# Kernel optimization log

Measured on AMD Instinct MI355X. Metric: run time of the kernel, lower is better.

Reference implementation:

```python
import jax, jax.numpy as jnp
import numpy as np

B, L = 256, 128            # batch_size, max_len
VOCAB, EMB = 50000, 448
POS_NUM, POS_SZ = 128, 32
UNITS = 512                # gru_units == EMB + 2*POS_SZ (BiGRU input dim)
NUM_CLASSES = 53


def setup_inputs() -> dict:
    key = jax.random.key(0)
    ks = jax.random.split(key, 16)
    s = 0.05
    return {
        "input_word": jax.random.randint(ks[0], (B, L), 0, VOCAB),
        "input_pos1": jax.random.randint(ks[1], (B, L), 0, POS_NUM),
        "input_pos2": jax.random.randint(ks[2], (B, L), 0, POS_NUM),
        "word_emb": jax.random.normal(ks[3], (VOCAB, EMB), jnp.float32) * s,
        "pos_emb": jax.random.normal(ks[4], (POS_NUM, POS_SZ), jnp.float32) * s,
        # Keras GRU (reset_after=True): kernel [D,3U], recurrent_kernel [U,3U], bias [2,3U]
        "gru_kernel_f": jax.random.normal(ks[5], (UNITS, 3 * UNITS), jnp.float32) * s,
        "gru_rkernel_f": jax.random.normal(ks[6], (UNITS, 3 * UNITS), jnp.float32) * s,
        "gru_bias_f": jax.random.normal(ks[7], (2, 3 * UNITS), jnp.float32) * s,
        "gru_kernel_b": jax.random.normal(ks[8], (UNITS, 3 * UNITS), jnp.float32) * s,
        "gru_rkernel_b": jax.random.normal(ks[9], (UNITS, 3 * UNITS), jnp.float32) * s,
        "gru_bias_b": jax.random.normal(ks[10], (2, 3 * UNITS), jnp.float32) * s,
        "attention_w": jax.random.normal(ks[11], (UNITS, 1), jnp.float32) * s,
        "sen_a": jax.random.normal(ks[12], (UNITS,), jnp.float32) * s,
        "sen_r": jax.random.normal(ks[13], (UNITS, 1), jnp.float32) * s,
        "sen_d": jax.random.normal(ks[14], (NUM_CLASSES,), jnp.float32) * s,
        "sen_s": jax.random.normal(ks[15], (NUM_CLASSES, UNITS), jnp.float32) * s,
    }


def _gru(x, kernel, rkernel, bias):
    """Keras GRU, reset_after=True, tanh/sigmoid activations. x: [B,L,D] -> [B,L,U]."""
    bi, br = bias[0], bias[1]
    # precompute input projections for all timesteps: [B,L,3U]
    xp = jnp.einsum('bld,dh->blh', x, kernel) + bi
    U = rkernel.shape[0]
    def step(h, xt):  # xt: [B,3U]
        rec = h @ rkernel + br
        xz, xr, xh = jnp.split(xt, 3, axis=-1)
        rz, rr, rh = jnp.split(rec, 3, axis=-1)
        z = jax.nn.sigmoid(xz + rz)
        r = jax.nn.sigmoid(xr + rr)
        hh = jnp.tanh(xh + r * rh)
        h_new = z * h + (1.0 - z) * hh
        return h_new, h_new
    h0 = jnp.zeros((x.shape[0], U), x.dtype)
    _, hs = jax.lax.scan(step, h0, jnp.swapaxes(xp, 0, 1))  # [L,B,U]
    return jnp.swapaxes(hs, 0, 1)


def _bigru(x, kf, rf, bf, kb, rb, bb):
    """Bidirectional GRU, merge_mode='sum'."""
    fwd = _gru(x, kf, rf, bf)
    bwd = _gru(x[:, ::-1], kb, rb, bb)[:, ::-1]
    return fwd + bwd


def reference(input_word, input_pos1, input_pos2, word_emb, pos_emb,
              gru_kernel_f, gru_rkernel_f, gru_bias_f,
              gru_kernel_b, gru_rkernel_b, gru_bias_b,
              attention_w, sen_a, sen_r, sen_d, sen_s):
    # embedding lookups; embedding of reversed indices == time-reverse of embedding
    we = word_emb[input_word]        # [B,L,EMB]
    p1 = pos_emb[input_pos1]         # [B,L,POS_SZ]
    p2 = pos_emb[input_pos2]
    x_f = jnp.concatenate([we, p1, p2], axis=-1)  # [B,L,UNITS]
    x_b = x_f[:, ::-1]
    # same BiGRU (shared weights) applied to forward and reversed inputs, summed
    h = (_bigru(x_f, gru_kernel_f, gru_rkernel_f, gru_bias_f,
                gru_kernel_b, gru_rkernel_b, gru_bias_b)
         + _bigru(x_b, gru_kernel_f, gru_rkernel_f, gru_bias_f,
                  gru_kernel_b, gru_rkernel_b, gru_bias_b))  # dropout = identity (inference)
    inputs_h = jnp.tanh(h)  # [B,L,U]
    # word attention: scalar score per token, softmax over sequence
    scores = (inputs_h @ attention_w)[..., 0]           # [B,L]
    w_alpha = jax.nn.softmax(scores, axis=-1)           # [B,L]
    w_att_r = jnp.einsum('bl,blu->bu', w_alpha, h)      # weighted sum of PRE-tanh h
    # sentence attention (vectorized over what was a per-sample Python loop)
    r = jnp.tanh(w_att_r)                               # [B,U]
    e = ((r * sen_a) @ sen_r)[:, 0]                     # [B]
    a = jax.nn.softmax(e, axis=0)[:, None]              # softmax across the batch, [B,1]
    s_c = a * r                                         # [B,U]
    logits = s_c @ sen_s.T + sen_d                      # [B,C]
    return jax.nn.softmax(logits, axis=-1)
```

## Files before the change

### kernel.cpp

```cpp
#include <hip/hip_runtime.h>
#include <cstddef>
#include <cstdint>

#define BATCH 256
#define SEQL  128
#define BL    (BATCH * SEQL)
#define DIM   512
#define N3    1536
#define NCLS  53
#define HGN   (4 * 256 * 512)

typedef float f32x4 __attribute__((ext_vector_type(4)));
typedef short s16x8 __attribute__((ext_vector_type(8)));
typedef short s16x4 __attribute__((ext_vector_type(4)));

__device__ __forceinline__ float bf2f(unsigned short u) {
    union { unsigned int i; float f; } v; v.i = ((unsigned int)u) << 16; return v.f;
}
__device__ __forceinline__ unsigned short f2bf(float f) {
    union { float f; unsigned int i; } v; v.f = f;
    unsigned int x = v.i;
    return (unsigned short)((x + 0x7fffu + ((x >> 16) & 1u)) >> 16);
}
__device__ __forceinline__ float wave_sum(float v) {
    #pragma unroll
    for (int m = 32; m > 0; m >>= 1) v += __shfl_xor(v, m);
    return v;
}
__device__ __forceinline__ float wave_max(float v) {
    #pragma unroll
    for (int m = 32; m > 0; m >>= 1) v = fmaxf(v, __shfl_xor(v, m));
    return v;
}
__device__ __forceinline__ float sigmoidf(float x) { return 1.0f / (1.0f + expf(-x)); }

__global__ __launch_bounds__(64) void zero_bar_kernel(int* bar) {
    bar[threadIdx.x * 32] = 0;
}

__global__ __launch_bounds__(256) void transpose_kernel(const float* __restrict__ W,
                                                        unsigned short* __restrict__ Wt) {
    __shared__ float tile[32][33];
    int tx = threadIdx.x & 31, ty = threadIdx.x >> 5;
    int n0 = blockIdx.x * 32, k0 = blockIdx.y * 32;
    #pragma unroll
    for (int r = 0; r < 4; ++r) {
        int kl = ty + r * 8;
        tile[kl][tx] = W[(size_t)(k0 + kl) * N3 + n0 + tx];
    }
    __syncthreads();
    #pragma unroll
    for (int r = 0; r < 4; ++r) {
        int nl = ty + r * 8;
        Wt[(size_t)(n0 + nl) * DIM + k0 + tx] = f2bf(tile[tx][nl]);
    }
}

__global__ __launch_bounds__(64) void gather_kernel(const int* __restrict__ iw,
                                                    const int* __restrict__ ip1,
                                                    const int* __restrict__ ip2,
                                                    const float* __restrict__ wemb,
                                                    const float* __restrict__ pemb,
                                                    unsigned short* __restrict__ X) {
    int row = blockIdx.x;
    int tid = threadIdx.x;
    int w = iw[row], p1 = ip1[row], p2 = ip2[row];
    int e0 = tid * 8;
    s16x8 o;
    #pragma unroll
    for (int j = 0; j < 8; ++j) {
        int e = e0 + j;
        float f;
        if (e < 448)      f = wemb[(size_t)w * 448 + e];
        else if (e < 480) f = pemb[p1 * 32 + (e - 448)];
        else              f = pemb[p2 * 32 + (e - 480)];
        o[j] = (short)f2bf(f);
    }
    *(s16x8*)(X + (size_t)row * DIM + e0) = o;
}

__global__ __launch_bounds__(256, 4) void xq_gemm_kernel(const unsigned short* __restrict__ X,
                                                         const unsigned short* __restrict__ Ktf,
                                                         const unsigned short* __restrict__ Ktb,
                                                         unsigned short* __restrict__ XQf,
                                                         unsigned short* __restrict__ XQb) {
    int dir = blockIdx.z & 1;
    int ns  = blockIdx.z >> 1;
    const unsigned short* Kt = dir ? Ktb : Ktf;
    unsigned short* XQ = dir ? XQb : XQf;
    int l    = blockIdx.x;
    int bblk = blockIdx.y;
    int b0 = bblk * 32;
    int u0 = ns * 128;

    __shared__ alignas(16) unsigned short As[32 * 512];
    int tid = threadIdx.x;
    #pragma unroll
    for (int it = 0; it < 8; ++it) {
        int lin = (it * 256 + tid) * 16;
        int row = lin >> 10;
        int off = lin & 1023;
        const char* src = (const char*)X + ((((size_t)(b0 + row)) * 128 + l) << 10) + off;
        *(s16x8*)((char*)As + (lin ^ ((row & 7) << 4))) = *(const s16x8*)src;
    }
    __syncthreads();

    int lane = tid & 63, wv = tid >> 6;
    int mi = wv >> 1, wc = wv & 1;
    int lr = lane & 15, lg = lane >> 4;

    f32x4 acc[3][4];
    #pragma unroll
    for (int g = 0; g < 3; ++g)
        #pragma unroll
        for (int ni = 0; ni < 4; ++ni) acc[g][ni] = (f32x4){0.f, 0.f, 0.f, 0.f};

    int ar = mi * 16 + lr;
    #pragma unroll 4
    for (int kk = 0; kk < 16; ++kk) {
        s16x8 a = *(const s16x8*)((const char*)As +
                    (((ar << 10) + (kk << 6) + (lg << 4)) ^ ((ar & 7) << 4)));
        #pragma unroll
        for (int g = 0; g < 3; ++g)
            #pragma unroll
            for (int ni = 0; ni < 4; ++ni) {
                int brow = g * 512 + u0 + wc * 64 + ni * 16 + lr;
                s16x8 b = *(const s16x8*)(Kt + ((size_t)brow << 9) + (kk << 5) + (lg << 3));
                acc[g][ni] = __builtin_amdgcn_mfma_f32_16x16x32_bf16(a, b, acc[g][ni], 0, 0, 0);
            }
    }

    int w_t = ns * 2 + wc;
    #pragma unroll
    for (int g = 0; g < 3; ++g)
        #pragma unroll
        for (int ni = 0; ni < 4; ++ni) {
            size_t base = (((size_t)l * 8 + bblk) * 8 + w_t) * 6144
                        + (size_t)((g * 4 + ni) * 2 + mi) * 256;
            s16x4 o;
            #pragma unroll
            for (int reg = 0; reg < 4; ++reg) o[reg] = (short)f2bf(acc[g][ni][reg]);
            *(s16x4*)(XQ + base + lane * 4) = o;
        }
}

__device__ __forceinline__ void group_barrier(int* cnt, int target) {
    __syncthreads();
    if (threadIdx.x == 0) {
        __hip_atomic_fetch_add(cnt, 1, __ATOMIC_RELEASE, __HIP_MEMORY_SCOPE_AGENT);
        while (__hip_atomic_load(cnt, __ATOMIC_RELAXED, __HIP_MEMORY_SCOPE_AGENT) < target)
            __builtin_amdgcn_s_sleep(1);
        __hip_atomic_fetch_add(cnt, 0, __ATOMIC_ACQUIRE, __HIP_MEMORY_SCOPE_AGENT);
    }
    __syncthreads();
}

__global__ __launch_bounds__(512, 2) void gru_coop2_kernel(
    const unsigned short* __restrict__ XQf, const unsigned short* __restrict__ XQb,
    const unsigned short* __restrict__ Btf, const unsigned short* __restrict__ Btb,
    const float* __restrict__ gbf, const float* __restrict__ gbb,
    unsigned short* __restrict__ Hg, int* __restrict__ bar,
    unsigned short* __restrict__ HA, unsigned short* __restrict__ HB,
    unsigned short* __restrict__ HC, unsigned short* __restrict__ HD) {
    int wg = blockIdx.x;
    int grp  = wg & 7;
    int run  = grp & 3;
    int rowh = grp >> 2;
    int uslc = wg >> 3;
    int* cnt = bar + grp * 32;
    const unsigned short* Bt = (run < 2) ? Btf : Btb;
    const unsigned short* XQ = (run < 2) ? XQf : XQb;
    const float* gb = (run < 2) ? gbf : gbb;
    unsigned short* Hout = (run == 0) ? HA : (run == 1) ? HB : (run == 2) ? HC : HD;
    bool revx = (run == 1 || run == 2);
    bool revo = (run >= 2);

    int tid = threadIdx.x;
    int lane = tid & 63, wv = tid >> 6;
    int lr = lane & 15, lg = lane >> 4;

    __shared__ alignas(16) unsigned short Ws[48 * 512];
    #pragma unroll
    for (int it = 0; it < 6; ++it) {
        int lin = (it * 512 + tid) * 16;
        int wrow = lin >> 10;
        int off = lin & 1023;
        int g = wrow >> 4, i = wrow & 15;
        const char* src = (const char*)Bt + (((size_t)(g * 512 + uslc * 16 + i)) << 10) + off;
        *(s16x8*)((char*)Ws + (lin ^ ((wrow & 7) << 4))) = *(const s16x8*)src;
    }

    int u_col = uslc * 16 + lr;
    float bZv  = gb[u_col] + gb[N3 + u_col];
    float bRv  = gb[512 + u_col] + gb[N3 + 512 + u_col];
    float bIHv = gb[1024 + u_col];
    float bRHv = gb[N3 + 1024 + u_col];

    int mrow0 = rowh * 128 + wv * 16;
    int arow  = mrow0 + lr;
    int bblk = rowh * 4 + (wv >> 1);
    int mi = wv & 1;
    int w_t = uslc >> 2, ni_t = uslc & 3;

    f32x4 hm = (f32x4){0.f, 0.f, 0.f, 0.f};
    #pragma unroll
    for (int reg = 0; reg < 4; ++reg) {
        int row = mrow0 + lg * 4 + reg;
        Hg[((size_t)(run * 256 + row) << 9) + u_col] = 0;
    }
    int target = 32;
    group_barrier(cnt, target); target += 32;

    for (int t = 0; t < SEQL; ++t) {
        const unsigned short* cur = Hg + (size_t)(t & 1) * HGN;
        unsigned short* nxt = Hg + (size_t)((t + 1) & 1) * HGN;
        int tx = revx ? (127 - t) : t;
        int th = revo ? (127 - t) : t;

        const unsigned short* xqb = XQ + (((size_t)tx * 8 + bblk) * 8 + w_t) * 6144
                                       + (size_t)lane * 4;
        s16x4 xqz = *(const s16x4*)(xqb + ((0 * 4 + ni_t) * 2 + mi) * 256);
        s16x4 xqr = *(const s16x4*)(xqb + ((1 * 4 + ni_t) * 2 + mi) * 256);
        s16x4 xqh = *(const s16x4*)(xqb + ((2 * 4 + ni_t) * 2 + mi) * 256);

        const unsigned short* ap = cur + ((size_t)(run * 256 + arow) << 9) + (lg << 3);

        f32x4 aZ = (f32x4){0.f, 0.f, 0.f, 0.f};
        f32x4 aR = (f32x4){0.f, 0.f, 0.f, 0.f};
        f32x4 aH = (f32x4){0.f, 0.f, 0.f, 0.f};
        const char* wsb = (const char*)Ws;
        #pragma unroll 8
        for (int kk = 0; kk < 16; ++kk) {
            s16x8 a = *(const s16x8*)(ap + (kk << 5));
            int sw = (lr & 7) << 4;
            s16x8 bz = *(const s16x8*)(wsb + ((((0 * 16 + lr) << 10) + (kk << 6) + (lg << 4)) ^ sw));
            s16x8 br = *(const s16x8*)(wsb + ((((1 * 16 + lr) << 10) + (kk << 6) + (lg << 4)) ^ sw));
            s16x8 bh = *(const s16x8*)(wsb + ((((2 * 16 + lr) << 10) + (kk << 6) + (lg << 4)) ^ sw));
            aZ = __builtin_amdgcn_mfma_f32_16x16x32_bf16(a, bz, aZ, 0, 0, 0);
            aR = __builtin_amdgcn_mfma_f32_16x16x32_bf16(a, br, aR, 0, 0, 0);
            aH = __builtin_amdgcn_mfma_f32_16x16x32_bf16(a, bh, aH, 0, 0, 0);
        }

        #pragma unroll
        for (int reg = 0; reg < 4; ++reg) {
            int row = mrow0 + lg * 4 + reg;
            float z  = sigmoidf(bf2f((unsigned short)xqz[reg]) + bZv + aZ[reg]);
            float rg = sigmoidf(bf2f((unsigned short)xqr[reg]) + bRv + aR[reg]);
            float hh = tanhf(bf2f((unsigned short)xqh[reg]) + bIHv + rg * (aH[reg] + bRHv));
            float hn = z * hm[reg] + (1.0f - z) * hh;
            hm[reg] = hn;
            unsigned short hb = f2bf(hn);
            nxt[((size_t)(run * 256 + row) << 9) + u_col] = hb;
            Hout[(((size_t)row * SEQL) + th) * DIM + u_col] = hb;
        }
        if (t < SEQL - 1) { group_barrier(cnt, target); target += 32; }
    }
}

__global__ __launch_bounds__(64) void attn_scores_kernel(const unsigned short* __restrict__ HA,
                                                         const unsigned short* __restrict__ HB,
                                                         const unsigned short* __restrict__ HC,
                                                         const unsigned short* __restrict__ HD,
                                                         const float* __restrict__ attw,
                                                         float* __restrict__ scores) {
    int bl = blockIdx.x;
    int lane = threadIdx.x;
    size_t base = (size_t)bl * DIM + lane * 8;
    s16x8 h1 = *(const s16x8*)(HA + base);
    s16x8 h2 = *(const s16x8*)(HB + base);
    s16x8 h3 = *(const s16x8*)(HC + base);
    s16x8 h4 = *(const s16x8*)(HD + base);
    float s = 0.0f;
    #pragma unroll
    for (int j = 0; j < 8; ++j) {
        float hv = bf2f((unsigned short)h1[j]) + bf2f((unsigned short)h2[j])
                 + bf2f((unsigned short)h3[j]) + bf2f((unsigned short)h4[j]);
        s += tanhf(hv) * attw[lane * 8 + j];
    }
    s = wave_sum(s);
    if (lane == 0) scores[bl] = s;
}

__global__ __launch_bounds__(64) void softmax_l_kernel(const float* __restrict__ scores,
                                                       float* __restrict__ alpha) {
    int b = blockIdx.x, lane = threadIdx.x;
    float s0 = scores[b * SEQL + lane];
    float s1 = scores[b * SEQL + 64 + lane];
    float m = wave_max(fmaxf(s0, s1));
    float e0 = expf(s0 - m), e1 = expf(s1 - m);
    float sum = wave_sum(e0 + e1);
    alpha[b * SEQL + lane] = e0 / sum;
    alpha[b * SEQL + 64 + lane] = e1 / sum;
}

__global__ __launch_bounds__(512) void attn_apply_kernel(const unsigned short* __restrict__ HA,
                                                         const unsigned short* __restrict__ HB,
                                                         const unsigned short* __restrict__ HC,
                                                         const unsigned short* __restrict__ HD,
                                                         const float* __restrict__ alpha,
                                                         const float* __restrict__ sena,
                                                         const float* __restrict__ senr,
                                                         float* __restrict__ rbuf,
                                                         float* __restrict__ ebuf) {
    int b = blockIdx.x, tid = threadIdx.x;
    __shared__ float al[SEQL];
    __shared__ float red[8];
    if (tid < SEQL) al[tid] = alpha[b * SEQL + tid];
    __syncthreads();
    float w0 = 0.0f;
    #pragma unroll 2
    for (int l = 0; l < SEQL; ++l) {
        size_t base = ((size_t)b * SEQL + l) * DIM + tid;
        w0 += al[l] * (bf2f(HA[base]) + bf2f(HB[base]) + bf2f(HC[base]) + bf2f(HD[base]));
    }
    float r0 = tanhf(w0);
    rbuf[(size_t)b * DIM + tid] = r0;
    float pv = r0 * sena[tid] * senr[tid];
    pv = wave_sum(pv);
    if ((tid & 63) == 0) red[tid >> 6] = pv;
    __syncthreads();
    if (tid == 0) {
        float s = 0.0f;
        #pragma unroll
        for (int i = 0; i < 8; ++i) s += red[i];
        ebuf[b] = s;
    }
}

__global__ __launch_bounds__(64) void batch_softmax_kernel(const float* __restrict__ ebuf,
                                                           float* __restrict__ abuf) {
    int lane = threadIdx.x;
    float v0 = ebuf[lane], v1 = ebuf[64 + lane], v2 = ebuf[128 + lane], v3 = ebuf[192 + lane];
    float m = wave_max(fmaxf(fmaxf(v0, v1), fmaxf(v2, v3)));
    float e0 = expf(v0 - m), e1 = expf(v1 - m), e2 = expf(v2 - m), e3 = expf(v3 - m);
    float s = wave_sum(e0 + e1 + e2 + e3);
    abuf[lane] = e0 / s; abuf[64 + lane] = e1 / s;
    abuf[128 + lane] = e2 / s; abuf[192 + lane] = e3 / s;
}

__global__ __launch_bounds__(64) void final_out_kernel(const float* __restrict__ rbuf,
                                                       const float* __restrict__ abuf,
                                                       const float* __restrict__ sens,
                                                       const float* __restrict__ send,
                                                       float* __restrict__ out) {
    int b = blockIdx.x, lane = threadIdx.x;
    __shared__ float lg[NCLS];
    float ab = abuf[b];
    float rv[8];
    #pragma unroll
    for (int j = 0; j < 8; ++j) rv[j] = rbuf[(size_t)b * DIM + j * 64 + lane];
    for (int c = 0; c < NCLS; ++c) {
        float d = 0.0f;
        #pragma unroll
        for (int j = 0; j < 8; ++j) d += rv[j] * sens[(size_t)c * DIM + j * 64 + lane];
        d = wave_sum(d);
        if (lane == 0) lg[c] = ab * d + send[c];
    }
    __syncthreads();
    float x = (lane < NCLS) ? lg[lane] : -3.0e38f;
    float m = wave_max(x);
    float ex = (lane < NCLS) ? expf(x - m) : 0.0f;
    float s = wave_sum(ex);
    if (lane < NCLS) out[b * NCLS + lane] = ex / s;
}

extern "C" void kernel_launch(void* const* d_in, const int* in_sizes, int n_in,
                              void* d_out, int out_size, void* d_ws, size_t ws_size,
                              hipStream_t stream) {
    (void)in_sizes; (void)n_in; (void)out_size; (void)ws_size;
    const int*   iw   = (const int*)d_in[0];
    const int*   ip1  = (const int*)d_in[1];
    const int*   ip2  = (const int*)d_in[2];
    const float* wemb = (const float*)d_in[3];
    const float* pemb = (const float*)d_in[4];
    const float* kf   = (const float*)d_in[5];
    const float* rf   = (const float*)d_in[6];
    const float* gbf  = (const float*)d_in[7];
    const float* kb   = (const float*)d_in[8];
    const float* rb   = (const float*)d_in[9];
    const float* gbb  = (const float*)d_in[10];
    const float* attw = (const float*)d_in[11];
    const float* sena = (const float*)d_in[12];
    const float* senr = (const float*)d_in[13];
    const float* send = (const float*)d_in[14];
    const float* sens = (const float*)d_in[15];
    float* out = (float*)d_out;

    char* p = (char*)d_ws;
    auto take = [&](size_t n) { char* q = p; p += ((n + 255) & ~(size_t)255); return q; };
    unsigned short* X    = (unsigned short*)take((size_t)BL * DIM * 2);
    unsigned short* Ktf  = (unsigned short*)take((size_t)N3 * DIM * 2);
    unsigned short* Ktb  = (unsigned short*)take((size_t)N3 * DIM * 2);
    unsigned short* Btf  = (unsigned short*)take((size_t)N3 * DIM * 2);
    unsigned short* Btb  = (unsigned short*)take((size_t)N3 * DIM * 2);
    unsigned short* XQf  = (unsigned short*)take((size_t)BL * N3 * 2);
    unsigned short* XQb  = (unsigned short*)take((size_t)BL * N3 * 2);
    unsigned short* HB   = (unsigned short*)take((size_t)BL * DIM * 2);
    unsigned short* HC   = (unsigned short*)take((size_t)BL * DIM * 2);
    unsigned short* HD   = (unsigned short*)take((size_t)BL * DIM * 2);
    unsigned short* Hg   = (unsigned short*)take((size_t)2 * HGN * 2);
    int*            bar  = (int*)take((size_t)64 * 32 * 4);
    float* scores = (float*)take((size_t)BL * 4);
    float* alpha  = (float*)take((size_t)BL * 4);
    float* rbuf   = (float*)take((size_t)BATCH * DIM * 4);
    float* ebuf   = (float*)take((size_t)BATCH * 4);
    float* abuf   = (float*)take((size_t)BATCH * 4);
    unsigned short* HA = X;

    zero_bar_kernel<<<1, 64, 0, stream>>>(bar);
    transpose_kernel<<<dim3(48, 16), 256, 0, stream>>>(kf, Ktf);
    transpose_kernel<<<dim3(48, 16), 256, 0, stream>>>(kb, Ktb);
    transpose_kernel<<<dim3(48, 16), 256, 0, stream>>>(rf, Btf);
    transpose_kernel<<<dim3(48, 16), 256, 0, stream>>>(rb, Btb);
    gather_kernel<<<BL, 64, 0, stream>>>(iw, ip1, ip2, wemb, pemb, X);

    xq_gemm_kernel<<<dim3(128, 8, 8), 256, 0, stream>>>(X, Ktf, Ktb, XQf, XQb);

    {
        const unsigned short* aXQf = XQf; const unsigned short* aXQb = XQb;
        const unsigned short* aBtf = Btf; const unsigned short* aBtb = Btb;
        const float* agbf = gbf; const float* agbb = gbb;
        unsigned short* aHg = Hg; int* abar = bar;
        unsigned short* aHA = HA; unsigned short* aHB = HB;
        unsigned short* aHC = HC; unsigned short* aHD = HD;
        void* args[] = { &aXQf, &aXQb, &aBtf, &aBtb, &agbf, &agbb,
                         &aHg, &abar, &aHA, &aHB, &aHC, &aHD };
        hipLaunchCooperativeKernel((void*)gru_coop2_kernel, dim3(256), dim3(512),
                                   args, 0, stream);
    }

    attn_scores_kernel<<<BL, 64, 0, stream>>>(HA, HB, HC, HD, attw, scores);
    softmax_l_kernel<<<BATCH, 64, 0, stream>>>(scores, alpha);
    attn_apply_kernel<<<BATCH, 512, 0, stream>>>(HA, HB, HC, HD, alpha, sena, senr, rbuf, ebuf);
    batch_softmax_kernel<<<1, 64, 0, stream>>>(ebuf, abuf);
    final_out_kernel<<<BATCH, 64, 0, stream>>>(rbuf, abuf, sens, send, out);
}
```

Baseline: 2.773 ms.

## Halve GRU block size, give each wave two M-tiles sharing B fragments

The cooperative GRU kernel now runs 256 threads per block instead of 512. Each wave computes two 16-row M tiles, so every LDS read of a recurrent-weight fragment feeds two MFMAs instead of one. The LDS weight layout is rewritten into a lane-major, MFMA-fragment order so each lane reads a contiguous 16-byte chunk without XOR swizzling. The intent is to cut LDS traffic and the per-block barrier cost, at the price of fewer waves to hide latency and more registers per thread.

```diff
diff --git a/kernel.cpp b/kernel.cpp
--- a/kernel.cpp
+++ b/kernel.cpp
@@ -155,7 +155,7 @@
     __syncthreads();
 }
 
-__global__ __launch_bounds__(512, 2) void gru_coop2_kernel(
+__global__ __launch_bounds__(256, 1) void gru_coop3_kernel(
     const unsigned short* __restrict__ XQf, const unsigned short* __restrict__ XQb,
     const unsigned short* __restrict__ Btf, const unsigned short* __restrict__ Btb,
     const float* __restrict__ gbf, const float* __restrict__ gbb,
@@ -181,13 +181,15 @@
 
     __shared__ alignas(16) unsigned short Ws[48 * 512];
     #pragma unroll
-    for (int it = 0; it < 6; ++it) {
-        int lin = (it * 512 + tid) * 16;
-        int wrow = lin >> 10;
-        int off = lin & 1023;
-        int g = wrow >> 4, i = wrow & 15;
-        const char* src = (const char*)Bt + (((size_t)(g * 512 + uslc * 16 + i)) << 10) + off;
-        *(s16x8*)((char*)Ws + (lin ^ ((wrow & 7) << 4))) = *(const s16x8*)src;
+    for (int it = 0; it < 12; ++it) {
+        int idx = it * 256 + tid;
+        int r  = idx & 15;
+        int lgs = (idx >> 4) & 3;
+        int kk = (idx >> 6) & 15;
+        int g  = idx >> 10;
+        const char* src = (const char*)Bt + (((size_t)(g * 512 + uslc * 16 + r)) << 10)
+                                          + (kk << 6) + (lgs << 4);
+        *(s16x8*)((char*)Ws + idx * 16) = *(const s16x8*)src;
     }
 
     int u_col = uslc * 16 + lr;
@@ -196,17 +198,17 @@
     float bIHv = gb[1024 + u_col];
     float bRHv = gb[N3 + 1024 + u_col];
 
-    int mrow0 = rowh * 128 + wv * 16;
-    int arow  = mrow0 + lr;
-    int bblk = rowh * 4 + (wv >> 1);
-    int mi = wv & 1;
+    int m0a = rowh * 128 + wv * 32;
+    int m0b = m0a + 16;
+    int bblk = rowh * 4 + wv;
     int w_t = uslc >> 2, ni_t = uslc & 3;
 
-    f32x4 hm = (f32x4){0.f, 0.f, 0.f, 0.f};
+    f32x4 hma = (f32x4){0.f, 0.f, 0.f, 0.f};
+    f32x4 hmb = (f32x4){0.f, 0.f, 0.f, 0.f};
     #pragma unroll
     for (int reg = 0; reg < 4; ++reg) {
-        int row = mrow0 + lg * 4 + reg;
-        Hg[((size_t)(run * 256 + row) << 9) + u_col] = 0;
+        Hg[((size_t)(run * 256 + m0a + lg * 4 + reg) << 9) + u_col] = 0;
+        Hg[((size_t)(run * 256 + m0b + lg * 4 + reg) << 9) + u_col] = 0;
     }
     int target = 32;
     group_barrier(cnt, target); target += 32;
@@ -219,39 +221,59 @@
 
         const unsigned short* xqb = XQ + (((size_t)tx * 8 + bblk) * 8 + w_t) * 6144
                                        + (size_t)lane * 4;
-        s16x4 xqz = *(const s16x4*)(xqb + ((0 * 4 + ni_t) * 2 + mi) * 256);
-        s16x4 xqr = *(const s16x4*)(xqb + ((1 * 4 + ni_t) * 2 + mi) * 256);
-        s16x4 xqh = *(const s16x4*)(xqb + ((2 * 4 + ni_t) * 2 + mi) * 256);
-
-        const unsigned short* ap = cur + ((size_t)(run * 256 + arow) << 9) + (lg << 3);
-
-        f32x4 aZ = (f32x4){0.f, 0.f, 0.f, 0.f};
-        f32x4 aR = (f32x4){0.f, 0.f, 0.f, 0.f};
-        f32x4 aH = (f32x4){0.f, 0.f, 0.f, 0.f};
-        const char* wsb = (const char*)Ws;
+        s16x4 xqza = *(const s16x4*)(xqb + ((0 * 4 + ni_t) * 2 + 0) * 256);
+        s16x4 xqzb = *(const s16x4*)(xqb + ((0 * 4 + ni_t) * 2 + 1) * 256);
+        s16x4 xqra = *(const s16x4*)(xqb + ((1 * 4 + ni_t) * 2 + 0) * 256);
+        s16x4 xqrb = *(const s16x4*)(xqb + ((1 * 4 + ni_t) * 2 + 1) * 256);
+        s16x4 xqha = *(const s16x4*)(xqb + ((2 * 4 + ni_t) * 2 + 0) * 256);
+        s16x4 xqhb = *(const s16x4*)(xqb + ((2 * 4 + ni_t) * 2 + 1) * 256);
+
+        const char* apa = (const char*)cur + (((size_t)(run * 256 + m0a + lr)) << 10) + (lg << 4);
+        const char* apb = (const char*)cur + (((size_t)(run * 256 + m0b + lr)) << 10) + (lg << 4);
+        const char* wsb = (const char*)Ws + (size_t)lane * 16;
+
+        f32x4 aZ0 = {0.f,0.f,0.f,0.f}, aZ1 = {0.f,0.f,0.f,0.f};
+        f32x4 aR0 = {0.f,0.f,0.f,0.f}, aR1 = {0.f,0.f,0.f,0.f};
+        f32x4 aH0 = {0.f,0.f,0.f,0.f}, aH1 = {0.f,0.f,0.f,0.f};
         #pragma unroll 8
         for (int kk = 0; kk < 16; ++kk) {
-            s16x8 a = *(const s16x8*)(ap + (kk << 5));
-            int sw = (lr & 7) << 4;
-            s16x8 bz = *(const s16x8*)(wsb + ((((0 * 16 + lr) << 10) + (kk << 6) + (lg << 4)) ^ sw));
-            s16x8 br = *(const s16x8*)(wsb + ((((1 * 16 + lr) << 10) + (kk << 6) + (lg << 4)) ^ sw));
-            s16x8 bh = *(const s16x8*)(wsb + ((((2 * 16 + lr) << 10) + (kk << 6) + (lg << 4)) ^ sw));
-            aZ = __builtin_amdgcn_mfma_f32_16x16x32_bf16(a, bz, aZ, 0, 0, 0);
-            aR = __builtin_amdgcn_mfma_f32_16x16x32_bf16(a, br, aR, 0, 0, 0);
-            aH = __builtin_amdgcn_mfma_f32_16x16x32_bf16(a, bh, aH, 0, 0, 0);
+            s16x8 a0 = *(const s16x8*)(apa + (kk << 6));
+            s16x8 a1 = *(const s16x8*)(apb + (kk << 6));
+            s16x8 bz = *(const s16x8*)(wsb + ((0 * 16 + kk) << 10));
+            s16x8 br = *(const s16x8*)(wsb + ((1 * 16 + kk) << 10));
+            s16x8 bh = *(const s16x8*)(wsb + ((2 * 16 + kk) << 10));
+            aZ0 = __builtin_amdgcn_mfma_f32_16x16x32_bf16(a0, bz, aZ0, 0, 0, 0);
+            aZ1 = __builtin_amdgcn_mfma_f32_16x16x32_bf16(a1, bz, aZ1, 0, 0, 0);
+            aR0 = __builtin_amdgcn_mfma_f32_16x16x32_bf16(a0, br, aR0, 0, 0, 0);
+            aR1 = __builtin_amdgcn_mfma_f32_16x16x32_bf16(a1, br, aR1, 0, 0, 0);
+            aH0 = __builtin_amdgcn_mfma_f32_16x16x32_bf16(a0, bh, aH0, 0, 0, 0);
+            aH1 = __builtin_amdgcn_mfma_f32_16x16x32_bf16(a1, bh, aH1, 0, 0, 0);
         }
 
         #pragma unroll
         for (int reg = 0; reg < 4; ++reg) {
-            int row = mrow0 + lg * 4 + reg;
-            float z  = sigmoidf(bf2f((unsigned short)xqz[reg]) + bZv + aZ[reg]);
-            float rg = sigmoidf(bf2f((unsigned short)xqr[reg]) + bRv + aR[reg]);
-            float hh = tanhf(bf2f((unsigned short)xqh[reg]) + bIHv + rg * (aH[reg] + bRHv));
-            float hn = z * hm[reg] + (1.0f - z) * hh;
-            hm[reg] = hn;
-            unsigned short hb = f2bf(hn);
-            nxt[((size_t)(run * 256 + row) << 9) + u_col] = hb;
-            Hout[(((size_t)row * SEQL) + th) * DIM + u_col] = hb;
+            {
+                int row = m0a + lg * 4 + reg;
+                float z  = sigmoidf(bf2f((unsigned short)xqza[reg]) + bZv + aZ0[reg]);
+                float rg = sigmoidf(bf2f((unsigned short)xqra[reg]) + bRv + aR0[reg]);
+                float hh = tanhf(bf2f((unsigned short)xqha[reg]) + bIHv + rg * (aH0[reg] + bRHv));
+                float hn = z * hma[reg] + (1.0f - z) * hh;
+                hma[reg] = hn;
+                unsigned short hb = f2bf(hn);
+                nxt[((size_t)(run * 256 + row) << 9) + u_col] = hb;
+                Hout[(((size_t)row * SEQL) + th) * DIM + u_col] = hb;
+            }
+            {
+                int row = m0b + lg * 4 + reg;
+                float z  = sigmoidf(bf2f((unsigned short)xqzb[reg]) + bZv + aZ1[reg]);
+                float rg = sigmoidf(bf2f((unsigned short)xqrb[reg]) + bRv + aR1[reg]);
+                float hh = tanhf(bf2f((unsigned short)xqhb[reg]) + bIHv + rg * (aH1[reg] + bRHv));
+                float hn = z * hmb[reg] + (1.0f - z) * hh;
+                hmb[reg] = hn;
+                unsigned short hb = f2bf(hn);
+                nxt[((size_t)(run * 256 + row) << 9) + u_col] = hb;
+                Hout[(((size_t)row * SEQL) + th) * DIM + u_col] = hb;
+            }
         }
         if (t < SEQL - 1) { group_barrier(cnt, target); target += 32; }
     }
@@ -425,7 +447,7 @@
         unsigned short* aHC = HC; unsigned short* aHD = HD;
         void* args[] = { &aXQf, &aXQb, &aBtf, &aBtb, &agbf, &agbb,
                          &aHg, &abar, &aHA, &aHB, &aHC, &aHD };
-        hipLaunchCooperativeKernel((void*)gru_coop2_kernel, dim3(256), dim3(512),
+        hipLaunchCooperativeKernel((void*)gru_coop3_kernel, dim3(256), dim3(256),
                                    args, 0, stream);
     }
 
```

Result: slower. 2.852 ms (+2.8%).

## Split GRU cooperative grid into smaller WGs, prefetch inputs across barrier

Applied to the files above, without the earlier changes.

The recurrent GRU kernel now launches 512 workgroups of 256 threads, split into 16 barrier groups of 32 workgroups that each own 64 batch rows, instead of 256 workgroups of 512 threads. Each thread now loads the next timestep's input projections before the group barrier and writes the per-timestep output after it, so both memory accesses overlap the barrier wait. The recurrent weight tile in shared memory is stored pre-permuted, so each lane reads it at a linear per-lane offset with no XOR swizzle. The barrier spin also sleeps longer per poll, which cuts atomic polling traffic but can add wake-up latency on every step.

```diff
diff --git a/kernel.cpp b/kernel.cpp
--- a/kernel.cpp
+++ b/kernel.cpp
@@ -34,8 +34,9 @@
 }
 __device__ __forceinline__ float sigmoidf(float x) { return 1.0f / (1.0f + expf(-x)); }
 
-__global__ __launch_bounds__(64) void zero_bar_kernel(int* bar) {
-    bar[threadIdx.x * 32] = 0;
+__global__ __launch_bounds__(256) void zero_bar_kernel(int* bar) {
+    #pragma unroll
+    for (int j = 0; j < 4; ++j) bar[threadIdx.x * 4 + j] = 0;
 }
 
 __global__ __launch_bounds__(256) void transpose_kernel(const float* __restrict__ W,
@@ -149,13 +150,13 @@
     if (threadIdx.x == 0) {
         __hip_atomic_fetch_add(cnt, 1, __ATOMIC_RELEASE, __HIP_MEMORY_SCOPE_AGENT);
         while (__hip_atomic_load(cnt, __ATOMIC_RELAXED, __HIP_MEMORY_SCOPE_AGENT) < target)
-            __builtin_amdgcn_s_sleep(1);
+            __builtin_amdgcn_s_sleep(8);
         __hip_atomic_fetch_add(cnt, 0, __ATOMIC_ACQUIRE, __HIP_MEMORY_SCOPE_AGENT);
     }
     __syncthreads();
 }
 
-__global__ __launch_bounds__(512, 2) void gru_coop2_kernel(
+__global__ __launch_bounds__(256, 2) void gru_coop4_kernel(
     const unsigned short* __restrict__ XQf, const unsigned short* __restrict__ XQb,
     const unsigned short* __restrict__ Btf, const unsigned short* __restrict__ Btb,
     const float* __restrict__ gbf, const float* __restrict__ gbb,
@@ -163,11 +164,11 @@
     unsigned short* __restrict__ HA, unsigned short* __restrict__ HB,
     unsigned short* __restrict__ HC, unsigned short* __restrict__ HD) {
     int wg = blockIdx.x;
-    int grp  = wg & 7;
+    int grp  = wg >> 5;
     int run  = grp & 3;
-    int rowh = grp >> 2;
-    int uslc = wg >> 3;
-    int* cnt = bar + grp * 32;
+    int rowq = grp >> 2;
+    int uslc = wg & 31;
+    int* cnt = bar + grp * 64;
     const unsigned short* Bt = (run < 2) ? Btf : Btb;
     const unsigned short* XQ = (run < 2) ? XQf : XQb;
     const float* gb = (run < 2) ? gbf : gbb;
@@ -181,13 +182,15 @@
 
     __shared__ alignas(16) unsigned short Ws[48 * 512];
     #pragma unroll
-    for (int it = 0; it < 6; ++it) {
-        int lin = (it * 512 + tid) * 16;
-        int wrow = lin >> 10;
-        int off = lin & 1023;
-        int g = wrow >> 4, i = wrow & 15;
-        const char* src = (const char*)Bt + (((size_t)(g * 512 + uslc * 16 + i)) << 10) + off;
-        *(s16x8*)((char*)Ws + (lin ^ ((wrow & 7) << 4))) = *(const s16x8*)src;
+    for (int it = 0; it < 12; ++it) {
+        int idx = it * 256 + tid;
+        int r  = idx & 15;
+        int lgs = (idx >> 4) & 3;
+        int kk = (idx >> 6) & 15;
+        int g  = idx >> 10;
+        const char* src = (const char*)Bt + (((size_t)(g * 512 + uslc * 16 + r)) << 10)
+                                          + (kk << 6) + (lgs << 4);
+        *(s16x8*)((char*)Ws + idx * 16) = *(const s16x8*)src;
     }
 
     int u_col = uslc * 16 + lr;
@@ -196,64 +199,77 @@
     float bIHv = gb[1024 + u_col];
     float bRHv = gb[N3 + 1024 + u_col];
 
-    int mrow0 = rowh * 128 + wv * 16;
-    int arow  = mrow0 + lr;
-    int bblk = rowh * 4 + (wv >> 1);
+    int m0 = rowq * 64 + wv * 16;
+    int bblk = rowq * 2 + (wv >> 1);
     int mi = wv & 1;
     int w_t = uslc >> 2, ni_t = uslc & 3;
 
     f32x4 hm = (f32x4){0.f, 0.f, 0.f, 0.f};
     #pragma unroll
-    for (int reg = 0; reg < 4; ++reg) {
-        int row = mrow0 + lg * 4 + reg;
-        Hg[((size_t)(run * 256 + row) << 9) + u_col] = 0;
-    }
+    for (int reg = 0; reg < 4; ++reg)
+        Hg[((size_t)(run * 256 + m0 + lg * 4 + reg) << 9) + u_col] = 0;
     int target = 32;
     group_barrier(cnt, target); target += 32;
+
+    int tx0 = revx ? 127 : 0;
+    const unsigned short* xqb0 = XQ + (((size_t)tx0 * 8 + bblk) * 8 + w_t) * 6144
+                                    + (size_t)lane * 4;
+    s16x4 xz = *(const s16x4*)(xqb0 + ((0 * 4 + ni_t) * 2 + mi) * 256);
+    s16x4 xr = *(const s16x4*)(xqb0 + ((1 * 4 + ni_t) * 2 + mi) * 256);
+    s16x4 xh = *(const s16x4*)(xqb0 + ((2 * 4 + ni_t) * 2 + mi) * 256);
 
     for (int t = 0; t < SEQL; ++t) {
         const unsigned short* cur = Hg + (size_t)(t & 1) * HGN;
         unsigned short* nxt = Hg + (size_t)((t + 1) & 1) * HGN;
-        int tx = revx ? (127 - t) : t;
         int th = revo ? (127 - t) : t;
 
-        const unsigned short* xqb = XQ + (((size_t)tx * 8 + bblk) * 8 + w_t) * 6144
-                                       + (size_t)lane * 4;
-        s16x4 xqz = *(const s16x4*)(xqb + ((0 * 4 + ni_t) * 2 + mi) * 256);
-        s16x4 xqr = *(const s16x4*)(xqb + ((1 * 4 + ni_t) * 2 + mi) * 256);
-        s16x4 xqh = *(const s16x4*)(xqb + ((2 * 4 + ni_t) * 2 + mi) * 256);
-
-        const unsigned short* ap = cur + ((size_t)(run * 256 + arow) << 9) + (lg << 3);
-
-        f32x4 aZ = (f32x4){0.f, 0.f, 0.f, 0.f};
-        f32x4 aR = (f32x4){0.f, 0.f, 0.f, 0.f};
-        f32x4 aH = (f32x4){0.f, 0.f, 0.f, 0.f};
-        const char* wsb = (const char*)Ws;
+        const char* ap = (const char*)cur + (((size_t)(run * 256 + m0 + lr)) << 10) + (lg << 4);
+        const char* wsb = (const char*)Ws + (size_t)lane * 16;
+
+        f32x4 aZ = {0.f,0.f,0.f,0.f};
+        f32x4 aR = {0.f,0.f,0.f,0.f};
+        f32x4 aH = {0.f,0.f,0.f,0.f};
         #pragma unroll 8
         for (int kk = 0; kk < 16; ++kk) {
-            s16x8 a = *(const s16x8*)(ap + (kk << 5));
-            int sw = (lr & 7) << 4;
-            s16x8 bz = *(const s16x8*)(wsb + ((((0 * 16 + lr) << 10) + (kk << 6) + (lg << 4)) ^ sw));
-            s16x8 br = *(const s16x8*)(wsb + ((((1 * 16 + lr) << 10) + (kk << 6) + (lg << 4)) ^ sw));
-            s16x8 bh = *(const s16x8*)(wsb + ((((2 * 16 + lr) << 10) + (kk << 6) + (lg << 4)) ^ sw));
+            s16x8 a  = *(const s16x8*)(ap + (kk << 6));
+            s16x8 bz = *(const s16x8*)(wsb + ((0 * 16 + kk) << 10));
+            s16x8 br = *(const s16x8*)(wsb + ((1 * 16 + kk) << 10));
+            s16x8 bh = *(const s16x8*)(wsb + ((2 * 16 + kk) << 10));
             aZ = __builtin_amdgcn_mfma_f32_16x16x32_bf16(a, bz, aZ, 0, 0, 0);
             aR = __builtin_amdgcn_mfma_f32_16x16x32_bf16(a, br, aR, 0, 0, 0);
             aH = __builtin_amdgcn_mfma_f32_16x16x32_bf16(a, bh, aH, 0, 0, 0);
         }
 
+        s16x4 pend;
         #pragma unroll
         for (int reg = 0; reg < 4; ++reg) {
-            int row = mrow0 + lg * 4 + reg;
-            float z  = sigmoidf(bf2f((unsigned short)xqz[reg]) + bZv + aZ[reg]);
-            float rg = sigmoidf(bf2f((unsigned short)xqr[reg]) + bRv + aR[reg]);
-            float hh = tanhf(bf2f((unsigned short)xqh[reg]) + bIHv + rg * (aH[reg] + bRHv));
+            int row = m0 + lg * 4 + reg;
+            float z  = sigmoidf(bf2f((unsigned short)xz[reg]) + bZv + aZ[reg]);
+            float rg = sigmoidf(bf2f((unsigned short)xr[reg]) + bRv + aR[reg]);
+            float hh = tanhf(bf2f((unsigned short)xh[reg]) + bIHv + rg * (aH[reg] + bRHv));
             float hn = z * hm[reg] + (1.0f - z) * hh;
             hm[reg] = hn;
             unsigned short hb = f2bf(hn);
+            pend[reg] = (short)hb;
             nxt[((size_t)(run * 256 + row) << 9) + u_col] = hb;
-            Hout[(((size_t)row * SEQL) + th) * DIM + u_col] = hb;
         }
-        if (t < SEQL - 1) { group_barrier(cnt, target); target += 32; }
+
+        if (t < SEQL - 1) {
+            int tx1 = revx ? (127 - (t + 1)) : (t + 1);
+            const unsigned short* xqb = XQ + (((size_t)tx1 * 8 + bblk) * 8 + w_t) * 6144
+                                           + (size_t)lane * 4;
+            s16x4 nz = *(const s16x4*)(xqb + ((0 * 4 + ni_t) * 2 + mi) * 256);
+            s16x4 nr = *(const s16x4*)(xqb + ((1 * 4 + ni_t) * 2 + mi) * 256);
+            s16x4 nh = *(const s16x4*)(xqb + ((2 * 4 + ni_t) * 2 + mi) * 256);
+            group_barrier(cnt, target); target += 32;
+            xz = nz; xr = nr; xh = nh;
+        }
+
+        #pragma unroll
+        for (int reg = 0; reg < 4; ++reg) {
+            int row = m0 + lg * 4 + reg;
+            Hout[(((size_t)row * SEQL) + th) * DIM + u_col] = (unsigned short)pend[reg];
+        }
     }
 }
 
@@ -399,7 +415,7 @@
     unsigned short* HC   = (unsigned short*)take((size_t)BL * DIM * 2);
     unsigned short* HD   = (unsigned short*)take((size_t)BL * DIM * 2);
     unsigned short* Hg   = (unsigned short*)take((size_t)2 * HGN * 2);
-    int*            bar  = (int*)take((size_t)64 * 32 * 4);
+    int*            bar  = (int*)take((size_t)1024 * 4);
     float* scores = (float*)take((size_t)BL * 4);
     float* alpha  = (float*)take((size_t)BL * 4);
     float* rbuf   = (float*)take((size_t)BATCH * DIM * 4);
@@ -407,7 +423,7 @@
     float* abuf   = (float*)take((size_t)BATCH * 4);
     unsigned short* HA = X;
 
-    zero_bar_kernel<<<1, 64, 0, stream>>>(bar);
+    zero_bar_kernel<<<1, 256, 0, stream>>>(bar);
     transpose_kernel<<<dim3(48, 16), 256, 0, stream>>>(kf, Ktf);
     transpose_kernel<<<dim3(48, 16), 256, 0, stream>>>(kb, Ktb);
     transpose_kernel<<<dim3(48, 16), 256, 0, stream>>>(rf, Btf);
@@ -425,7 +441,7 @@
         unsigned short* aHC = HC; unsigned short* aHD = HD;
         void* args[] = { &aXQf, &aXQb, &aBtf, &aBtb, &agbf, &agbb,
                          &aHg, &abar, &aHA, &aHB, &aHC, &aHD };
-        hipLaunchCooperativeKernel((void*)gru_coop2_kernel, dim3(256), dim3(512),
+        hipLaunchCooperativeKernel((void*)gru_coop4_kernel, dim3(512), dim3(256),
                                    args, 0, stream);
     }
 
```

After: 4.566 ms. +64.7%, slower.
